# Kernel optimization log

Measured on AMD Instinct MI355X. Metric: run time of the kernel, lower is better.

## Reference

```python
import jax, jax.numpy as jnp
import numpy as np

B, S, D, H = 2, 2048, 1024, 16
DK = D // H
ALPHA = 0.3


def setup_inputs() -> dict:
    key = jax.random.key(0)
    ks = jax.random.split(key, 10)
    w = 0.02  # weight init scale
    return {
        "z_real": jax.random.normal(ks[0], (B, S, D), jnp.float32),
        "z_imag": jax.random.normal(ks[1], (B, S, D), jnp.float32),
        # weights stored [in, out]; applied as x @ W (equivalent to torch Linear with weight W.T)
        "Wq_r": jax.random.normal(ks[2], (D, D), jnp.float32) * w,
        "Wq_i": jax.random.normal(ks[3], (D, D), jnp.float32) * w,
        "Wk_r": jax.random.normal(ks[4], (D, D), jnp.float32) * w,
        "Wk_i": jax.random.normal(ks[5], (D, D), jnp.float32) * w,
        "Wv": jax.random.normal(ks[6], (D, D), jnp.float32) * w,
        "Wo_w": jax.random.normal(ks[7], (D, D), jnp.float32) * w,
        "Wo_b": jnp.zeros((D,), jnp.float32),
        "mask": jax.random.randint(ks[8], (B, S), 0, 2, jnp.int32),
    }


def _heads(x):
    # [B,S,D] -> [B,S,H,DK]
    return x.reshape(B, S, H, DK)


def reference(z_real, z_imag, Wq_r, Wq_i, Wk_r, Wk_i, Wv, Wo_w, Wo_b, mask):
    scale = 1.0 / np.sqrt(DK)
    # complex projections: Q = (Wq_r + i Wq_i)(z_real + i z_imag), same for K
    Qr = _heads(z_real @ Wq_r - z_imag @ Wq_i)
    Qi = _heads(z_imag @ Wq_r + z_real @ Wq_i)
    Kr = _heads(z_real @ Wk_r - z_imag @ Wk_i)
    Ki = _heads(z_imag @ Wk_r + z_real @ Wk_i)
    V = _heads(z_real @ Wv)
    # scores = Q K^H * scale; real/imag parts without complex dtype
    Sr = (jnp.einsum('bqhd,bkhd->bhqk', Qr, Kr)
          + jnp.einsum('bqhd,bkhd->bhqk', Qi, Ki)) * scale
    Si = (jnp.einsum('bqhd,bkhd->bhqk', Qi, Kr)
          - jnp.einsum('bqhd,bkhd->bhqk', Qr, Ki)) * scale
    # variant == 'hybrid': (|s| + alpha*cos(angle(s))) / sqrt(d_k)
    mag = jnp.sqrt(Sr * Sr + Si * Si)
    cos_phase = Sr / mag  # cos(angle(s)) = Re(s)/|s|
    scores = (mag + ALPHA * cos_phase) * scale
    # key-padding mask [B,S] -> [B,1,1,S]
    scores = jnp.where(mask[:, None, None, :] == 0, -1e9, scores)
    probs = jax.nn.softmax(scores, axis=-1)  # dropout inactive (eval)
    context = jnp.einsum('bhqk,bkhd->bqhd', probs, V).reshape(B, S, D)
    out = context @ Wo_w + Wo_b
    return out, probs.mean(axis=1)
```

## Files before the change

kernel.cpp:

```cpp
#include <hip/hip_runtime.h>
#include <cstdint>
#include <cstddef>

#define BB 2
#define SS 2048
#define DD 1024
#define HH 16
#define DKK 64

typedef __attribute__((ext_vector_type(8))) short short8x;
typedef __attribute__((ext_vector_type(4))) float f32x4;

__device__ __forceinline__ unsigned short f2b(float f) {
  union { float f; unsigned u; } v; v.f = f;
  unsigned r = (v.u + 0x7fffu + ((v.u >> 16) & 1u)) >> 16;
  return (unsigned short)r;
}

__device__ __forceinline__ unsigned short f2b_fast(float f) {
  union { float f; unsigned u; } v; v.f = f;
  return (unsigned short)((v.u + 0x8000u) >> 16);
}

__device__ __forceinline__ f32x4 mfma16(short8x a, short8x b, f32x4 c) {
  return __builtin_amdgcn_mfma_f32_16x16x32_bf16(a, b, c, 0, 0, 0);
}

__device__ __forceinline__ void gload16(const unsigned short* g, unsigned short* l) {
  __builtin_amdgcn_global_load_lds(
      (__attribute__((address_space(1))) unsigned int*)g,
      (__attribute__((address_space(3))) unsigned int*)l,
      16, 0, 0);
}

#define C1F 0.0225421076f
#define C2F 0.0541010849f

__global__ __launch_bounds__(256) void pack_w_kernel(
    const float* __restrict__ Wq_r, const float* __restrict__ Wq_i,
    const float* __restrict__ Wk_r, const float* __restrict__ Wk_i,
    const float* __restrict__ Wv, const float* __restrict__ Wo,
    unsigned short* __restrict__ WcatT, unsigned short* __restrict__ WoT) {
  __shared__ float tile[64][65];
  const int tid = threadIdx.x;
  int bid = blockIdx.x;
  if (bid < 2560) {
    const int kt = bid & 31, nt = bid >> 5;
    const int k0 = kt * 64, n0 = nt * 64;
    const int q = n0 >> 10, j0 = n0 & 1023;
    const float* src;
    float sgn = 1.0f;
    bool zero = false;
    if (k0 < 1024) {
      src = (q == 0) ? Wq_r : (q == 1) ? Wq_i : (q == 2) ? Wk_r : (q == 3) ? Wk_i : Wv;
    } else {
      if (q == 0)      { src = Wq_i; sgn = -1.0f; }
      else if (q == 1) { src = Wq_r; }
      else if (q == 2) { src = Wk_i; sgn = -1.0f; }
      else if (q == 3) { src = Wk_r; }
      else             { src = Wv; zero = true; }
    }
    const int ks0 = k0 & 1023;
    if (!zero) {
#pragma unroll
      for (int i = 0; i < 16; i++) {
        int idx = i * 256 + tid;
        int r = idx >> 6, c = idx & 63;
        tile[r][c] = src[(size_t)(ks0 + r) * 1024 + j0 + c];
      }
      __syncthreads();
#pragma unroll
      for (int i = 0; i < 16; i++) {
        int idx = i * 256 + tid;
        int nr = idx >> 6, kc = idx & 63;
        WcatT[(size_t)(n0 + nr) * 2048 + k0 + kc] = f2b(sgn * tile[kc][nr]);
      }
    } else {
#pragma unroll
      for (int i = 0; i < 16; i++) {
        int idx = i * 256 + tid;
        int nr = idx >> 6, kc = idx & 63;
        WcatT[(size_t)(n0 + nr) * 2048 + k0 + kc] = 0;
      }
    }
  } else {
    bid -= 2560;
    const int kt = bid & 15, nt = bid >> 4;
    const int k0 = kt * 64, n0 = nt * 64;
#pragma unroll
    for (int i = 0; i < 16; i++) {
      int idx = i * 256 + tid;
      int r = idx >> 6, c = idx & 63;
      tile[r][c] = Wo[(size_t)(k0 + r) * 1024 + n0 + c];
    }
    __syncthreads();
#pragma unroll
    for (int i = 0; i < 16; i++) {
      int idx = i * 256 + tid;
      int nr = idx >> 6, kc = idx & 63;
      WoT[(size_t)(n0 + nr) * 1024 + k0 + kc] = f2b(tile[kc][nr]);
    }
  }
}

__global__ void pack_x_kernel(const float* __restrict__ zr, const float* __restrict__ zi,
                              unsigned short* __restrict__ X) {
  int gid = blockIdx.x * 256 + threadIdx.x;
  int k8 = (gid & 255) << 3;
  int m = gid >> 8;
  const float* src = (k8 < 1024) ? (zr + (size_t)m * 1024 + k8)
                                 : (zi + (size_t)m * 1024 + (k8 - 1024));
  float4 a = *(const float4*)src;
  float4 c = *(const float4*)(src + 4);
  ushort4 o0; o0.x = f2b(a.x); o0.y = f2b(a.y); o0.z = f2b(a.z); o0.w = f2b(a.w);
  ushort4 o1; o1.x = f2b(c.x); o1.y = f2b(c.y); o1.z = f2b(c.z); o1.w = f2b(c.w);
  *(ushort4*)(X + (size_t)gid * 8) = o0;
  *(ushort4*)(X + (size_t)gid * 8 + 4) = o1;
}

__global__ void zero_kernel(float4* __restrict__ p) {
  p[(size_t)blockIdx.x * 256 + threadIdx.x] = float4{0.f, 0.f, 0.f, 0.f};
}

__global__ void mask_scan_kernel(const int* __restrict__ mask,
                                 unsigned short* __restrict__ pos,
                                 unsigned short* __restrict__ idx,
                                 int* __restrict__ cnt) {
  const int b = blockIdx.x >> 1, half = blockIdx.x & 1;
  __shared__ int sums[256];
  const int t = threadIdx.x;
  const int s0 = half * 1024 + t * 4;
  int m[4];
  int loc = 0;
#pragma unroll
  for (int i = 0; i < 4; i++) { m[i] = mask[b * 2048 + s0 + i]; loc += m[i]; }
  sums[t] = loc;
  __syncthreads();
  for (int off = 1; off < 256; off <<= 1) {
    int v = (t >= off) ? sums[t - off] : 0;
    __syncthreads();
    sums[t] += v;
    __syncthreads();
  }
  int excl = sums[t] - loc;
#pragma unroll
  for (int i = 0; i < 4; i++) {
    int sg = s0 + i;
    if (m[i]) {
      pos[b * 2048 + sg] = (unsigned short)excl;
      idx[(b * 2 + half) * 1024 + excl] = (unsigned short)sg;
      excl++;
    } else {
      pos[b * 2048 + sg] = 0xFFFFu;
    }
  }
  if (t == 255) cnt[b * 2 + half] = sums[255];
}

__global__ __launch_bounds__(256, 5) void gemm_proj_kernel(
    const unsigned short* __restrict__ A, const unsigned short* __restrict__ Bt,
    const unsigned short* __restrict__ pos,
    unsigned short* __restrict__ Qr, unsigned short* __restrict__ Qi,
    unsigned short* __restrict__ Kr, unsigned short* __restrict__ Ki,
    unsigned short* __restrict__ VT) {
  constexpr int K = 2048;
  __shared__ __attribute__((aligned(16))) unsigned short As[128][32];
  __shared__ __attribute__((aligned(16))) unsigned short Bs[128][32];
  const int tid = threadIdx.x;
  const int m0 = blockIdx.x * 128;
  const int n0 = blockIdx.y * 128;
  const int lane = tid & 63, wid = tid >> 6;
  const int l15 = lane & 15, quad = lane >> 4;
  const int wm = (wid & 1) * 64, wn = (wid >> 1) * 64;
  const int r4 = lane >> 2, c8 = (lane & 3) * 8;
  const int kmax = (n0 >= 4096) ? 1024 : K;
  f32x4 acc[4][4] = {};
  const unsigned short* pa0 = A + (size_t)(m0 + wid * 16 + r4) * K + c8;
  const unsigned short* pa1 = pa0 + (size_t)64 * K;
  const unsigned short* pb0 = Bt + (size_t)(n0 + wid * 16 + r4) * K + c8;
  const unsigned short* pb1 = pb0 + (size_t)64 * K;
  unsigned short* la0 = &As[wid * 16][0];
  unsigned short* la1 = &As[64 + wid * 16][0];
  unsigned short* lb0 = &Bs[wid * 16][0];
  unsigned short* lb1 = &Bs[64 + wid * 16][0];
  for (int k0 = 0; k0 < kmax; k0 += 32) {
    __syncthreads();
    gload16(pa0, la0);  gload16(pa1, la1);
    gload16(pb0, lb0);  gload16(pb1, lb1);
    pa0 += 32; pa1 += 32; pb0 += 32; pb1 += 32;
    __syncthreads();
    short8x af[4], bfr[4];
#pragma unroll
    for (int i = 0; i < 4; i++) af[i]  = *(const short8x*)&As[wm + i * 16 + l15][quad * 8];
#pragma unroll
    for (int i = 0; i < 4; i++) bfr[i] = *(const short8x*)&Bs[wn + i * 16 + l15][quad * 8];
#pragma unroll
    for (int mi = 0; mi < 4; mi++)
#pragma unroll
      for (int ni = 0; ni < 4; ni++)
        acc[mi][ni] = mfma16(af[mi], bfr[ni], acc[mi][ni]);
  }
#pragma unroll
  for (int mi = 0; mi < 4; mi++) {
#pragma unroll
    for (int ni = 0; ni < 4; ni++) {
      int gn = n0 + wn + ni * 16 + l15;
      if (gn < 2048) {
        int which = gn >> 10, j = gn & 1023, h = j >> 6, dk = j & 63;
        int ks = dk >> 5, q = (dk >> 3) & 3, e = dk & 7;
        unsigned short* dst = which ? Qi : Qr;
#pragma unroll
        for (int r = 0; r < 4; r++) {
          int gm = m0 + wm + mi * 16 + quad * 4 + r;
          int b = gm >> 11, s = gm & 2047;
          int bh = b * HH + h, rb = s >> 4, l = s & 15;
          dst[(size_t)(((bh * 128 + rb) * 2 + ks) * 512 + (q * 16 + l) * 8 + e)] = f2b(acc[mi][ni][r]);
        }
      } else if (gn < 4096) {
        int which = gn >> 10, j = gn & 1023, h = j >> 6, dk = j & 63;
        int ks = dk >> 5, q = (dk >> 3) & 3, e = dk & 7;
        unsigned short* dst = (which == 2) ? Kr : Ki;
#pragma unroll
        for (int r = 0; r < 4; r++) {
          int gm = m0 + wm + mi * 16 + quad * 4 + r;
          int b = gm >> 11, s = gm & 2047;
          unsigned short pp = pos[b * 2048 + s];
          if (pp != 0xFFFFu) {
            int hf = s >> 10;
            int bh = b * HH + h, rb = hf * 64 + (pp >> 4), l = pp & 15;
            dst[(size_t)(((bh * 128 + rb) * 2 + ks) * 512 + (q * 16 + l) * 8 + e)] = f2b(acc[mi][ni][r]);
          }
        }
      } else {
        int j = gn - 4096, h = j >> 6, dk = j & 63;
        int rbv = dk >> 4, lv = dk & 15;
#pragma unroll
        for (int r = 0; r < 4; r++) {
          int gm = m0 + wm + mi * 16 + quad * 4 + r;
          int b = gm >> 11, s = gm & 2047;
          unsigned short pp = pos[b * 2048 + s];
          if (pp != 0xFFFFu) {
            int hf = s >> 10;
            int bh = b * HH + h, kc = hf * 32 + (pp >> 5), qv = (pp >> 3) & 3, ev = pp & 7;
            VT[(size_t)(((bh * 4 + rbv) * 64 + kc) * 512 + (qv * 16 + lv) * 8 + ev)] = f2b(acc[mi][ni][r]);
          }
        }
      }
    }
  }
}

__global__ __launch_bounds__(256, 4) void flash_kernel(
    const unsigned short* __restrict__ Qr, const unsigned short* __restrict__ Qi,
    const unsigned short* __restrict__ Kr, const unsigned short* __restrict__ Ki,
    const unsigned short* __restrict__ VT, const int* __restrict__ cnt,
    float* __restrict__ ctxP0, float* __restrict__ ctxP1,
    float* __restrict__ Lp0, float* __restrict__ Lp1) {
  __shared__ __attribute__((aligned(16))) unsigned short Ps[2][4][16][72];
  __shared__ __attribute__((aligned(16))) unsigned short Ks[2][4][2][512];
  const int tid = threadIdx.x;
  const int lane = tid & 63, wid = tid >> 6;
  const int l15 = lane & 15, quad = lane >> 4;
  int lin = blockIdx.x + 16 * (blockIdx.y + 16 * blockIdx.z);
  lin = ((lin & 7) << 7) | (lin >> 3);
  const int qt2 = (lin & 15) * 128;
  const int h = (lin >> 4) & 15;
  const int z = lin >> 8;
  const int b = z >> 1, half = z & 1;
  const int bh = b * HH + h;
  float* __restrict__ cp = half ? ctxP1 : ctxP0;
  float* __restrict__ lp = half ? Lp1 : Lp0;
  const int cntbh = cnt[b * 2 + half];
  const int kend = ((cntbh + 63) >> 6) << 6;
  const int kt0 = half * 1024;

  short8x fqr0[2], fqr1[2], fqi0[2], fqi1[2];
#pragma unroll
  for (int s2 = 0; s2 < 2; s2++) {
    const int rb = ((qt2 + s2 * 64) >> 4) + wid;
    const int qb = (bh * 128 + rb) * 1024 + lane * 8;
    fqr0[s2] = *(const short8x*)(Qr + qb);
    fqr1[s2] = *(const short8x*)(Qr + qb + 512);
    fqi0[s2] = *(const short8x*)(Qi + qb);
    fqi1[s2] = *(const short8x*)(Qi + qb + 512);
  }
  f32x4 ctxacc[2][4] = {};
  float lsum[2][4] = {{0.f, 0.f, 0.f, 0.f}, {0.f, 0.f, 0.f, 0.f}};

  const int sf0 = wid * 4;

  for (int ktl = 0; ktl < kend; ktl += 64) {
    const int kt = kt0 + ktl;
    const int rbb = bh * 128 + (kt >> 4);
    __syncthreads();
#pragma unroll
    for (int fi = 0; fi < 4; fi++) {
      int f = sf0 + fi;
      int arr = f >> 3, rbl = (f >> 1) & 3, ks = f & 1;
      const unsigned short* src = (arr ? Ki : Kr) + ((size_t)(rbb + rbl) * 2 + ks) * 512 + lane * 8;
      gload16(src, &Ks[arr][rbl][ks][0]);
    }
    __syncthreads();
#pragma unroll
    for (int nb = 0; nb < 4; nb++) {
      const int j = ktl + nb * 16 + l15;
      short8x bkr0 = *(const short8x*)&Ks[0][nb][0][lane * 8];
      short8x bkr1 = *(const short8x*)&Ks[0][nb][1][lane * 8];
      short8x bki0 = *(const short8x*)&Ks[1][nb][0][lane * 8];
      short8x bki1 = *(const short8x*)&Ks[1][nb][1][lane * 8];
#pragma unroll
      for (int s2 = 0; s2 < 2; s2++) {
        f32x4 sr = {0.f, 0.f, 0.f, 0.f};
        sr = mfma16(fqr0[s2], bkr0, sr);  sr = mfma16(fqr1[s2], bkr1, sr);
        sr = mfma16(fqi0[s2], bki0, sr);  sr = mfma16(fqi1[s2], bki1, sr);
        f32x4 sa = {0.f, 0.f, 0.f, 0.f};
        sa = mfma16(fqi0[s2], bkr0, sa);  sa = mfma16(fqi1[s2], bkr1, sa);
        f32x4 sb = {0.f, 0.f, 0.f, 0.f};
        sb = mfma16(fqr0[s2], bki0, sb);  sb = mfma16(fqr1[s2], bki1, sb);
#pragma unroll
        for (int r = 0; r < 4; r++) {
          float a = sr[r];
          float d = sa[r] - sb[r];
          float r2 = __builtin_fmaf(a, a, d * d);
          float inv = __builtin_amdgcn_rsqf(r2);
          float arg = inv * __builtin_fmaf(C1F, r2, C2F * a);
          float p = (j < cntbh) ? __builtin_amdgcn_exp2f(arg) : 0.0f;
          lsum[s2][r] += p;
          Ps[s2][wid][quad * 4 + r][nb * 16 + l15] = f2b_fast(p);
        }
      }
    }
#pragma unroll
    for (int ks = 0; ks < 2; ks++)
#pragma unroll
      for (int db = 0; db < 4; db++) {
        int voff = ((bh * 4 + db) * 64 + (kt >> 5) + ks) * 512 + lane * 8;
        short8x bv = *(const short8x*)(VT + voff);
        short8x ap0 = *(const short8x*)&Ps[0][wid][l15][ks * 32 + quad * 8];
        short8x ap1 = *(const short8x*)&Ps[1][wid][l15][ks * 32 + quad * 8];
        ctxacc[0][db] = mfma16(ap0, bv, ctxacc[0][db]);
        ctxacc[1][db] = mfma16(ap1, bv, ctxacc[1][db]);
      }
  }
#pragma unroll
  for (int s2 = 0; s2 < 2; s2++) {
#pragma unroll
    for (int r = 0; r < 4; r++) {
#pragma unroll
      for (int off = 1; off < 16; off <<= 1) lsum[s2][r] += __shfl_xor(lsum[s2][r], off, 64);
    }
#pragma unroll
    for (int r = 0; r < 4; r++) {
      int s = qt2 + s2 * 64 + wid * 16 + quad * 4 + r;
#pragma unroll
      for (int db = 0; db < 4; db++)
        cp[((size_t)b * SS + s) * DD + h * DKK + db * 16 + l15] = ctxacc[s2][db][r];
      if (l15 == 0) lp[(size_t)bh * SS + s] = lsum[s2][r];
    }
  }
}

__global__ __launch_bounds__(256) void combine_kernel(
    const float* __restrict__ ctxP0, const float* __restrict__ ctxP1,
    const float* __restrict__ Lp0, const float* __restrict__ Lp1,
    unsigned short* __restrict__ ctx) {
  int idx = blockIdx.x * 256 + threadIdx.x;
  int g = idx * 4;
  int c = g & 1023, s = (g >> 10) & 2047, b = g >> 21;
  int h = c >> 6;
  size_t loff = (size_t)(b * HH + h) * SS + s;
  float linv = 1.0f / (Lp0[loff] + Lp1[loff]);
  float4 p0 = *(const float4*)(ctxP0 + g);
  float4 p1 = *(const float4*)(ctxP1 + g);
  ushort4 o;
  o.x = f2b((p0.x + p1.x) * linv);
  o.y = f2b((p0.y + p1.y) * linv);
  o.z = f2b((p0.z + p1.z) * linv);
  o.w = f2b((p0.w + p1.w) * linv);
  *(ushort4*)(ctx + g) = o;
}

__global__ __launch_bounds__(256, 2) void gemm_out_kernel(
    const unsigned short* __restrict__ A, const unsigned short* __restrict__ Bt,
    const float* __restrict__ bias, float* __restrict__ out) {
  constexpr int K = 1024;
  __shared__ __attribute__((aligned(16))) unsigned short As[64][32];
  __shared__ __attribute__((aligned(16))) unsigned short Bs[128][32];
  const int tid = threadIdx.x;
  const int m0 = blockIdx.x * 64;
  const int n0 = blockIdx.y * 128;
  const int lane = tid & 63, wid = tid >> 6;
  const int l15 = lane & 15, quad = lane >> 4;
  const int wm = (wid & 1) * 32, wn = (wid >> 1) * 64;
  const int r4 = lane >> 2, c8 = (lane & 3) * 8;
  f32x4 acc[2][4] = {};
  const unsigned short* pa0 = A + (size_t)(m0 + wid * 16 + r4) * K + c8;
  const unsigned short* pb0 = Bt + (size_t)(n0 + wid * 16 + r4) * K + c8;
  const unsigned short* pb1 = pb0 + (size_t)64 * K;
  unsigned short* la0 = &As[wid * 16][0];
  unsigned short* lb0 = &Bs[wid * 16][0];
  unsigned short* lb1 = &Bs[64 + wid * 16][0];
  for (int k0 = 0; k0 < K; k0 += 32) {
    __syncthreads();
    gload16(pa0, la0);
    gload16(pb0, lb0);  gload16(pb1, lb1);
    pa0 += 32; pb0 += 32; pb1 += 32;
    __syncthreads();
    short8x af[2], bfr[4];
#pragma unroll
    for (int i = 0; i < 2; i++) af[i]  = *(const short8x*)&As[wm + i * 16 + l15][quad * 8];
#pragma unroll
    for (int i = 0; i < 4; i++) bfr[i] = *(const short8x*)&Bs[wn + i * 16 + l15][quad * 8];
#pragma unroll
    for (int mi = 0; mi < 2; mi++)
#pragma unroll
      for (int ni = 0; ni < 4; ni++)
        acc[mi][ni] = mfma16(af[mi], bfr[ni], acc[mi][ni]);
  }
#pragma unroll
  for (int mi = 0; mi < 2; mi++)
#pragma unroll
    for (int ni = 0; ni < 4; ni++) {
      int gn = n0 + wn + ni * 16 + l15;
      float bv = bias[gn];
#pragma unroll
      for (int r = 0; r < 4; r++) {
        int gm = m0 + wm + mi * 16 + quad * 4 + r;
        out[(size_t)gm * 1024 + gn] = acc[mi][ni][r] + bv;
      }
    }
}

__global__ __launch_bounds__(256, 4) void probsmean_kernel(
    const unsigned short* __restrict__ Qr, const unsigned short* __restrict__ Qi,
    const unsigned short* __restrict__ Kr, const unsigned short* __restrict__ Ki,
    const int* __restrict__ cnt, const unsigned short* __restrict__ idxT,
    const float* __restrict__ Lp0, const float* __restrict__ Lp1,
    float* __restrict__ out2) {
  __shared__ __attribute__((aligned(16))) unsigned short Ks[2][4][2][512];
  const int tid = threadIdx.x, lane = tid & 63, wid = tid >> 6;
  const int l15 = lane & 15, quad = lane >> 4;
  const int qt = blockIdx.x * 64;
  const int b = blockIdx.z;
  const int c0 = cnt[b * 2], c1 = cnt[b * 2 + 1];
  const int t0n = (c0 + 63) >> 6;
  const int t1n = (c1 + 63) >> 6;
  const int t = blockIdx.y;
  int half, jl0, cnth;
  if (t < t0n)            { half = 0; jl0 = t * 64;         cnth = c0; }
  else if (t < t0n + t1n) { half = 1; jl0 = (t - t0n) * 64; cnth = c1; }
  else return;
  const int qrow0 = qt + wid * 16;
  const int qrb = (qt >> 4) + wid;
  const int ktb = half * 64 + (jl0 >> 4);
  const int sf0 = wid * 4;
  int korig[4]; bool vld[4];
#pragma unroll
  for (int nb = 0; nb < 4; nb++) {
    int j = jl0 + nb * 16 + l15;
    vld[nb] = j < cnth;
    korig[nb] = idxT[(b * 2 + half) * 1024 + j];
  }
  float psum[4][4] = {};
  for (int h = 0; h < HH; h++) {
    const int bh = b * HH + h;
    const int qoff = (bh * 128 + qrb) * 1024 + lane * 8;
    short8x fqr0 = *(const short8x*)(Qr + qoff);
    short8x fqr1 = *(const short8x*)(Qr + qoff + 512);
    short8x fqi0 = *(const short8x*)(Qi + qoff);
    short8x fqi1 = *(const short8x*)(Qi + qoff + 512);
    const float4 lv0 = *(const float4*)(Lp0 + (size_t)bh * SS + qrow0 + quad * 4);
    const float4 lv1 = *(const float4*)(Lp1 + (size_t)bh * SS + qrow0 + quad * 4);
    float li[4];
    li[0] = 1.0f / (lv0.x + lv1.x); li[1] = 1.0f / (lv0.y + lv1.y);
    li[2] = 1.0f / (lv0.z + lv1.z); li[3] = 1.0f / (lv0.w + lv1.w);
    const int rbb = bh * 128 + ktb;
    __syncthreads();
#pragma unroll
    for (int fi = 0; fi < 4; fi++) {
      int f = sf0 + fi;
      int arr = f >> 3, rbl = (f >> 1) & 3, ks = f & 1;
      const unsigned short* src = (arr ? Ki : Kr) + ((size_t)(rbb + rbl) * 2 + ks) * 512 + lane * 8;
      gload16(src, &Ks[arr][rbl][ks][0]);
    }
    __syncthreads();
#pragma unroll
    for (int nb = 0; nb < 4; nb++) {
      short8x bkr0 = *(const short8x*)&Ks[0][nb][0][lane * 8];
      short8x bkr1 = *(const short8x*)&Ks[0][nb][1][lane * 8];
      short8x bki0 = *(const short8x*)&Ks[1][nb][0][lane * 8];
      short8x bki1 = *(const short8x*)&Ks[1][nb][1][lane * 8];
      f32x4 sr = {0.f, 0.f, 0.f, 0.f};
      sr = mfma16(fqr0, bkr0, sr);  sr = mfma16(fqr1, bkr1, sr);
      sr = mfma16(fqi0, bki0, sr);  sr = mfma16(fqi1, bki1, sr);
      f32x4 sa = {0.f, 0.f, 0.f, 0.f};
      sa = mfma16(fqi0, bkr0, sa);  sa = mfma16(fqi1, bkr1, sa);
      f32x4 sb = {0.f, 0.f, 0.f, 0.f};
      sb = mfma16(fqr0, bki0, sb);  sb = mfma16(fqr1, bki1, sb);
#pragma unroll
      for (int r = 0; r < 4; r++) {
        float a = sr[r];
        float d = sa[r] - sb[r];
        float r2 = __builtin_fmaf(a, a, d * d);
        float inv = __builtin_amdgcn_rsqf(r2);
        float arg = inv * __builtin_fmaf(C1F, r2, C2F * a);
        float p = vld[nb] ? __builtin_amdgcn_exp2f(arg) * li[r] : 0.0f;
        psum[nb][r] += p;
      }
    }
  }
#pragma unroll
  for (int nb = 0; nb < 4; nb++)
#pragma unroll
    for (int r = 0; r < 4; r++) {
      if (vld[nb]) {
        int qrow = qrow0 + quad * 4 + r;
        out2[((size_t)b * SS + qrow) * SS + korig[nb]] = psum[nb][r] * 0.0625f;
      }
    }
}

extern "C" void kernel_launch(void* const* d_in, const int* in_sizes, int n_in,
                              void* d_out, int out_size, void* d_ws, size_t ws_size,
                              hipStream_t stream) {
  const float* z_real = (const float*)d_in[0];
  const float* z_imag = (const float*)d_in[1];
  const float* Wq_r = (const float*)d_in[2];
  const float* Wq_i = (const float*)d_in[3];
  const float* Wk_r = (const float*)d_in[4];
  const float* Wk_i = (const float*)d_in[5];
  const float* Wv   = (const float*)d_in[6];
  const float* Wo_w = (const float*)d_in[7];
  const float* Wo_b = (const float*)d_in[8];
  const int*   mask = (const int*)d_in[9];
  char* ws = (char*)d_ws;

  constexpr size_t QKV_BYTES = 8388608;
  unsigned short* Qr   = (unsigned short*)(ws + 0);
  unsigned short* Qi   = (unsigned short*)(ws + QKV_BYTES);
  unsigned short* Kr   = (unsigned short*)(ws + 2 * QKV_BYTES);
  unsigned short* Ki   = (unsigned short*)(ws + 3 * QKV_BYTES);
  unsigned short* VT   = (unsigned short*)(ws + 4 * QKV_BYTES);
  unsigned short* ctx  = (unsigned short*)(ws + 5 * QKV_BYTES);
  unsigned short* WcatT= (unsigned short*)(ws + 50331648);
  unsigned short* WoT  = (unsigned short*)(ws + 71303168);
  unsigned short* Xcat = (unsigned short*)(ws + 73400320);
  float* ctxP0 = (float*)(ws + 50331648);
  float* ctxP1 = (float*)(ws + 73400320);
  float* Lp0   = (float*)(ws + 90177536);
  float* Lp1   = (float*)(ws + 90439680);

  float* out  = (float*)d_out;
  float* out2 = out + (size_t)BB * SS * DD;

  unsigned short* posT = (unsigned short*)out;
  unsigned short* idxT = posT + 4096;
  int* cntT = (int*)(idxT + 4096);

  pack_w_kernel<<<dim3(2816), dim3(256), 0, stream>>>(Wq_r, Wq_i, Wk_r, Wk_i, Wv, Wo_w, WcatT, WoT);
  pack_x_kernel<<<dim3(4096), dim3(256), 0, stream>>>(z_real, z_imag, Xcat);
  zero_kernel<<<dim3(2048), dim3(256), 0, stream>>>((float4*)VT);
  zero_kernel<<<dim3(8192), dim3(256), 0, stream>>>((float4*)out2);
  mask_scan_kernel<<<dim3(4), dim3(256), 0, stream>>>(mask, posT, idxT, cntT);
  gemm_proj_kernel<<<dim3(32, 40), dim3(256), 0, stream>>>(Xcat, WcatT, posT, Qr, Qi, Kr, Ki, VT);
  flash_kernel<<<dim3(16, 16, 4), dim3(256), 0, stream>>>(Qr, Qi, Kr, Ki, VT, cntT, ctxP0, ctxP1, Lp0, Lp1);
  probsmean_kernel<<<dim3(32, 32, 2), dim3(256), 0, stream>>>(Qr, Qi, Kr, Ki, cntT, idxT, Lp0, Lp1, out2);
  combine_kernel<<<dim3(4096), dim3(256), 0, stream>>>(ctxP0, ctxP1, Lp0, Lp1, ctx);
  gemm_out_kernel<<<dim3(64, 8), dim3(256), 0, stream>>>(ctx, WoT, Wo_b, out);
}
```

Before: 397.3 us.

## Compact unmasked rows for K/V projection and skip fully masked GEMM tiles

The pack kernel now also writes a compacted copy of the input containing only unmasked sequence rows, grouped by batch and half, into the out2 buffer used as scratch. The K/V part of the projection GEMM reads this compacted copy and returns early for row tiles beyond the valid count, so no MFMA work is spent on masked keys. The epilogue no longer looks up pos per row. In exchange the pack kernel does extra scattered writes, and the mask scan and the out2 zeroing are reordered so the scratch buffer is used before it gets cleared.

```diff
diff --git a/kernel.cpp b/kernel.cpp
--- a/kernel.cpp
+++ b/kernel.cpp
@@ -104,7 +104,9 @@
 }
 
 __global__ void pack_x_kernel(const float* __restrict__ zr, const float* __restrict__ zi,
-                              unsigned short* __restrict__ X) {
+                              const unsigned short* __restrict__ pos,
+                              unsigned short* __restrict__ X,
+                              unsigned short* __restrict__ Xc2) {
   int gid = blockIdx.x * 256 + threadIdx.x;
   int k8 = (gid & 255) << 3;
   int m = gid >> 8;
@@ -116,6 +118,13 @@
   ushort4 o1; o1.x = f2b(c.x); o1.y = f2b(c.y); o1.z = f2b(c.z); o1.w = f2b(c.w);
   *(ushort4*)(X + (size_t)gid * 8) = o0;
   *(ushort4*)(X + (size_t)gid * 8 + 4) = o1;
+  unsigned short pp = pos[m];
+  if (pp != 0xFFFFu) {
+    int b = m >> 11, s = m & 2047, half = s >> 10;
+    size_t drow = (size_t)((b * 2 + half) * 1024 + pp);
+    *(ushort4*)(Xc2 + drow * 2048 + k8) = o0;
+    *(ushort4*)(Xc2 + drow * 2048 + k8 + 4) = o1;
+  }
 }
 
 __global__ void zero_kernel(float4* __restrict__ p) {
@@ -158,24 +167,31 @@
 }
 
 __global__ __launch_bounds__(256, 5) void gemm_proj_kernel(
-    const unsigned short* __restrict__ A, const unsigned short* __restrict__ Bt,
-    const unsigned short* __restrict__ pos,
+    const unsigned short* __restrict__ A, const unsigned short* __restrict__ Ac,
+    const unsigned short* __restrict__ Bt, const int* __restrict__ cnt,
     unsigned short* __restrict__ Qr, unsigned short* __restrict__ Qi,
     unsigned short* __restrict__ Kr, unsigned short* __restrict__ Ki,
     unsigned short* __restrict__ VT) {
   constexpr int K = 2048;
+  const int n0 = blockIdx.y * 128;
+  const bool qpath = (n0 < 2048);
+  const int m0 = blockIdx.x * 128;
+  int cntg = 0;
+  if (!qpath) {
+    cntg = cnt[blockIdx.x >> 3];
+    if (((blockIdx.x & 7) * 128) >= cntg) return;
+  }
   __shared__ __attribute__((aligned(16))) unsigned short As[128][32];
   __shared__ __attribute__((aligned(16))) unsigned short Bs[128][32];
   const int tid = threadIdx.x;
-  const int m0 = blockIdx.x * 128;
-  const int n0 = blockIdx.y * 128;
   const int lane = tid & 63, wid = tid >> 6;
   const int l15 = lane & 15, quad = lane >> 4;
   const int wm = (wid & 1) * 64, wn = (wid >> 1) * 64;
   const int r4 = lane >> 2, c8 = (lane & 3) * 8;
   const int kmax = (n0 >= 4096) ? 1024 : K;
   f32x4 acc[4][4] = {};
-  const unsigned short* pa0 = A + (size_t)(m0 + wid * 16 + r4) * K + c8;
+  const unsigned short* Ab = qpath ? A : Ac;
+  const unsigned short* pa0 = Ab + (size_t)(m0 + wid * 16 + r4) * K + c8;
   const unsigned short* pa1 = pa0 + (size_t)64 * K;
   const unsigned short* pb0 = Bt + (size_t)(n0 + wid * 16 + r4) * K + c8;
   const unsigned short* pb1 = pb0 + (size_t)64 * K;
@@ -200,12 +216,12 @@
       for (int ni = 0; ni < 4; ni++)
         acc[mi][ni] = mfma16(af[mi], bfr[ni], acc[mi][ni]);
   }
-#pragma unroll
-  for (int mi = 0; mi < 4; mi++) {
-#pragma unroll
-    for (int ni = 0; ni < 4; ni++) {
-      int gn = n0 + wn + ni * 16 + l15;
-      if (gn < 2048) {
+  if (qpath) {
+#pragma unroll
+    for (int mi = 0; mi < 4; mi++)
+#pragma unroll
+      for (int ni = 0; ni < 4; ni++) {
+        int gn = n0 + wn + ni * 16 + l15;
         int which = gn >> 10, j = gn & 1023, h = j >> 6, dk = j & 63;
         int ks = dk >> 5, q = (dk >> 3) & 3, e = dk & 7;
         unsigned short* dst = which ? Qi : Qr;
@@ -216,37 +232,42 @@
           int bh = b * HH + h, rb = s >> 4, l = s & 15;
           dst[(size_t)(((bh * 128 + rb) * 2 + ks) * 512 + (q * 16 + l) * 8 + e)] = f2b(acc[mi][ni][r]);
         }
-      } else if (gn < 4096) {
-        int which = gn >> 10, j = gn & 1023, h = j >> 6, dk = j & 63;
-        int ks = dk >> 5, q = (dk >> 3) & 3, e = dk & 7;
-        unsigned short* dst = (which == 2) ? Kr : Ki;
-#pragma unroll
-        for (int r = 0; r < 4; r++) {
-          int gm = m0 + wm + mi * 16 + quad * 4 + r;
-          int b = gm >> 11, s = gm & 2047;
-          unsigned short pp = pos[b * 2048 + s];
-          if (pp != 0xFFFFu) {
-            int hf = s >> 10;
-            int bh = b * HH + h, rb = hf * 64 + (pp >> 4), l = pp & 15;
-            dst[(size_t)(((bh * 128 + rb) * 2 + ks) * 512 + (q * 16 + l) * 8 + e)] = f2b(acc[mi][ni][r]);
+      }
+  } else {
+    const int g = blockIdx.x >> 3;
+    const int b = g >> 1, hf = g & 1;
+#pragma unroll
+    for (int mi = 0; mi < 4; mi++)
+#pragma unroll
+      for (int ni = 0; ni < 4; ni++) {
+        int gn = n0 + wn + ni * 16 + l15;
+        if (gn < 4096) {
+          int which = gn >> 10, j = gn & 1023, h = j >> 6, dk = j & 63;
+          int ks = dk >> 5, q = (dk >> 3) & 3, e = dk & 7;
+          unsigned short* dst = (which == 2) ? Kr : Ki;
+#pragma unroll
+          for (int r = 0; r < 4; r++) {
+            int gm = m0 + wm + mi * 16 + quad * 4 + r;
+            int local = gm & 1023;
+            if (local < cntg) {
+              int bh = b * HH + h, rb = hf * 64 + (local >> 4), l = local & 15;
+              dst[(size_t)(((bh * 128 + rb) * 2 + ks) * 512 + (q * 16 + l) * 8 + e)] = f2b(acc[mi][ni][r]);
+            }
+          }
+        } else {
+          int j = gn - 4096, h = j >> 6, dk = j & 63;
+          int rbv = dk >> 4, lv = dk & 15;
+#pragma unroll
+          for (int r = 0; r < 4; r++) {
+            int gm = m0 + wm + mi * 16 + quad * 4 + r;
+            int local = gm & 1023;
+            if (local < cntg) {
+              int bh = b * HH + h, kc = hf * 32 + (local >> 5), qv = (local >> 3) & 3, ev = local & 7;
+              VT[(size_t)(((bh * 4 + rbv) * 64 + kc) * 512 + (qv * 16 + lv) * 8 + ev)] = f2b(acc[mi][ni][r]);
+            }
           }
         }
-      } else {
-        int j = gn - 4096, h = j >> 6, dk = j & 63;
-        int rbv = dk >> 4, lv = dk & 15;
-#pragma unroll
-        for (int r = 0; r < 4; r++) {
-          int gm = m0 + wm + mi * 16 + quad * 4 + r;
-          int b = gm >> 11, s = gm & 2047;
-          unsigned short pp = pos[b * 2048 + s];
-          if (pp != 0xFFFFu) {
-            int hf = s >> 10;
-            int bh = b * HH + h, kc = hf * 32 + (pp >> 5), qv = (pp >> 3) & 3, ev = pp & 7;
-            VT[(size_t)(((bh * 4 + rbv) * 64 + kc) * 512 + (qv * 16 + lv) * 8 + ev)] = f2b(acc[mi][ni][r]);
-          }
-        }
-      }
-    }
+      }
   }
 }
 
@@ -556,13 +577,14 @@
   unsigned short* posT = (unsigned short*)out;
   unsigned short* idxT = posT + 4096;
   int* cntT = (int*)(idxT + 4096);
-
+  unsigned short* Xc2 = (unsigned short*)out2;
+
+  mask_scan_kernel<<<dim3(4), dim3(256), 0, stream>>>(mask, posT, idxT, cntT);
   pack_w_kernel<<<dim3(2816), dim3(256), 0, stream>>>(Wq_r, Wq_i, Wk_r, Wk_i, Wv, Wo_w, WcatT, WoT);
-  pack_x_kernel<<<dim3(4096), dim3(256), 0, stream>>>(z_real, z_imag, Xcat);
+  pack_x_kernel<<<dim3(4096), dim3(256), 0, stream>>>(z_real, z_imag, posT, Xcat, Xc2);
   zero_kernel<<<dim3(2048), dim3(256), 0, stream>>>((float4*)VT);
+  gemm_proj_kernel<<<dim3(32, 40), dim3(256), 0, stream>>>(Xcat, Xc2, WcatT, cntT, Qr, Qi, Kr, Ki, VT);
   zero_kernel<<<dim3(8192), dim3(256), 0, stream>>>((float4*)out2);
-  mask_scan_kernel<<<dim3(4), dim3(256), 0, stream>>>(mask, posT, idxT, cntT);
-  gemm_proj_kernel<<<dim3(32, 40), dim3(256), 0, stream>>>(Xcat, WcatT, posT, Qr, Qi, Kr, Ki, VT);
   flash_kernel<<<dim3(16, 16, 4), dim3(256), 0, stream>>>(Qr, Qi, Kr, Ki, VT, cntT, ctxP0, ctxP1, Lp0, Lp1);
   probsmean_kernel<<<dim3(32, 32, 2), dim3(256), 0, stream>>>(Qr, Qi, Kr, Ki, cntT, idxT, Lp0, Lp1, out2);
   combine_kernel<<<dim3(4096), dim3(256), 0, stream>>>(ctxP0, ctxP1, Lp0, Lp1, ctx);
```

Result: faster. 373.0 us (-6.1%).
